# Optimization experiments

Hardware: AMD Instinct MI355X
Metric: run time of the kernel (lower is better)

Reference implementation:

```python
import jax, jax.numpy as jnp
import numpy as np

N_SKILLS = 1024
HIDDEN = 512
BATCH = 64
SEQ = 512
INPUT_DIM = 2 * N_SKILLS


def _lstm_layer(x_tbd, W_ih, W_hh, b_ih, b_hh):
    # x_tbd: [S, B, D_in]; PyTorch gate order: i, f, g, o
    B = x_tbd.shape[1]
    H = W_hh.shape[1]
    h0 = jnp.zeros((B, H), x_tbd.dtype)
    c0 = jnp.zeros((B, H), x_tbd.dtype)

    def step(carry, xt):
        h, c = carry
        gates = xt @ W_ih.T + h @ W_hh.T + (b_ih + b_hh)
        i, f, g, o = jnp.split(gates, 4, axis=-1)
        c_new = jax.nn.sigmoid(f) * c + jax.nn.sigmoid(i) * jnp.tanh(g)
        h_new = jax.nn.sigmoid(o) * jnp.tanh(c_new)
        return (h_new, c_new), h_new

    _, hs = jax.lax.scan(step, (h0, c0), x_tbd)
    return hs  # [S, B, H]


def setup_inputs() -> dict:
    key = jax.random.key(0)
    ks = jax.random.split(key, 12)
    s = 1.0 / np.sqrt(HIDDEN)  # PyTorch LSTM init scale
    inp = {
        "skills": jax.random.randint(ks[0], (BATCH, SEQ), 0, N_SKILLS, dtype=jnp.int32),
        "corrects": jax.random.randint(ks[1], (BATCH, SEQ), 0, 2, dtype=jnp.int32),
        # LSTM layer 0: input_dim = 2*n_skills
        "W_ih0": jax.random.uniform(ks[2], (4 * HIDDEN, INPUT_DIM), jnp.float32, -s, s),
        "W_hh0": jax.random.uniform(ks[3], (4 * HIDDEN, HIDDEN), jnp.float32, -s, s),
        "b_ih0": jax.random.uniform(ks[4], (4 * HIDDEN,), jnp.float32, -s, s),
        "b_hh0": jax.random.uniform(ks[5], (4 * HIDDEN,), jnp.float32, -s, s),
        # LSTM layer 1: input = hidden
        "W_ih1": jax.random.uniform(ks[6], (4 * HIDDEN, HIDDEN), jnp.float32, -s, s),
        "W_hh1": jax.random.uniform(ks[7], (4 * HIDDEN, HIDDEN), jnp.float32, -s, s),
        "b_ih1": jax.random.uniform(ks[8], (4 * HIDDEN,), jnp.float32, -s, s),
        "b_hh1": jax.random.uniform(ks[9], (4 * HIDDEN,), jnp.float32, -s, s),
        # Output projection
        "fc_W": jax.random.uniform(ks[10], (N_SKILLS, HIDDEN), jnp.float32, -s, s),
        "fc_b": jax.random.uniform(ks[11], (N_SKILLS,), jnp.float32, -s, s),
    }
    return inp


def reference(skills, corrects, W_ih0, W_hh0, b_ih0, b_hh0,
              W_ih1, W_hh1, b_ih1, b_hh1, fc_W, fc_b):
    # Vectorized one-hot encoding: index = skill if correct==1 else n_skills+skill
    idx = skills + N_SKILLS * (1 - (corrects == 1).astype(skills.dtype))
    valid = (skills >= 0)
    x = jax.nn.one_hot(idx, INPUT_DIM, dtype=jnp.float32) * valid[..., None]  # [B,S,2n]

    x = jnp.transpose(x, (1, 0, 2))  # [S, B, 2n]
    h1 = _lstm_layer(x, W_ih0, W_hh0, b_ih0, b_hh0)   # [S, B, H]
    h2 = _lstm_layer(h1, W_ih1, W_hh1, b_ih1, b_hh1)  # [S, B, H]
    rnn_out = jnp.transpose(h2, (1, 0, 2))  # [B, S, H]

    # dropout is identity at inference
    logits = rnn_out @ fc_W.T + fc_b  # [B, S, n_skills]
    return jax.nn.sigmoid(logits)
```

## Files before the change

### kernel.cpp

```cpp
#include <hip/hip_runtime.h>
#include <hip/hip_fp16.h>

typedef _Float16 f16;
typedef unsigned int u32;
typedef unsigned long long u64;
typedef _Float16 f16x4 __attribute__((ext_vector_type(4)));
typedef _Float16 f16x8 __attribute__((ext_vector_type(8)));
typedef float f32x4 __attribute__((ext_vector_type(4)));
typedef float f32x16 __attribute__((ext_vector_type(16)));

#define SEQ   512
#define HID   512
#define NSK   1024
#define INDIM 2048
#define G4    2048
#define NWG   64
#define TWORDS 8192

#define H1_OFF    0ull
#define H2_OFF    33554432ull
#define WHH0_OFF  67108864ull
#define WIH1_OFF  69206016ull
#define WHH1_OFF  71303168ull
#define FCW_OFF   73400320ull
#define B0_OFF    74448896ull
#define B1_OFF    74457088ull
#define W0P_OFF   74465280ull
#define FLG_OFF   82853888ull

__device__ __forceinline__ float sigmoidf_(float x) {
    return 1.0f / (1.0f + __expf(-x));
}
__device__ __forceinline__ float tanhf_(float x) {
    return 2.0f * sigmoidf_(2.0f * x) - 1.0f;
}

__device__ __forceinline__ void cstore(u64* p, u64 v) {
    __hip_atomic_store(p, v, __ATOMIC_RELAXED, __HIP_MEMORY_SCOPE_AGENT);
}

__global__ __launch_bounds__(256) void prep_kernel(
    const float* __restrict__ Whh0, const float* __restrict__ Wih1,
    const float* __restrict__ Whh1, const float* __restrict__ fcW,
    const float* __restrict__ bih0, const float* __restrict__ bhh0,
    const float* __restrict__ bih1, const float* __restrict__ bhh1,
    f16* __restrict__ whh0h, f16* __restrict__ wih1h,
    f16* __restrict__ whh1h, f16* __restrict__ fcwh,
    float* __restrict__ b0, float* __restrict__ b1, u32* __restrict__ flags)
{
    int i = blockIdx.x * 256 + threadIdx.x;
    if (i < G4 * HID) {
        whh0h[i] = (f16)Whh0[i];
        wih1h[i] = (f16)Wih1[i];
        whh1h[i] = (f16)Whh1[i];
    }
    if (i < NSK * HID) fcwh[i] = (f16)fcW[i];
    if (i < G4) { b0[i] = bih0[i] + bhh0[i]; b1[i] = bih1[i] + bhh1[i]; }
    if (i < NWG * 16) flags[i] = 0;
}

__global__ __launch_bounds__(256) void w0p_kernel(
    const float* __restrict__ Wih0, f16* __restrict__ w0p)
{
    __shared__ float tl[64][65];
    const int tid = threadIdx.x;
    const int ct = blockIdx.x & 31, rt = blockIdx.x >> 5;
    const int r0 = rt * 64, c0 = ct * 64;
#pragma unroll 4
    for (int i = 0; i < 16; ++i) {
        int rr = i * 4 + (tid >> 6);
        int cc = tid & 63;
        tl[rr][cc] = Wih0[(size_t)(r0 + rr) * INDIM + c0 + cc];
    }
    __syncthreads();
    const int jh = r0 >> 9;
    const int wg0 = (r0 & 511) >> 3;
    for (int task = tid; task < 512; task += 256) {
        int c = task >> 3, wgl = task & 7;
        f16 tmp[8];
#pragma unroll
        for (int jl = 0; jl < 8; ++jl) tmp[jl] = (f16)tl[wgl * 8 + jl][c];
        *(f16x8*)&w0p[(size_t)(c0 + c) * 2048 + (wg0 + wgl) * 32 + jh * 8] =
            *(f16x8*)tmp;
    }
}

struct PArgs {
    const int* skills; const int* corrects;
    const f16* W0P;
    const f16* Whh0; const f16* Wih1; const f16* Whh1;
    const float* b0; const float* b1;
    u64* h1; u64* h2;
    u32* arrive;
};

__global__ __launch_bounds__(256, 1) void lstm_mfma(PArgs a) {
    __shared__ float ex[2 * 2 * 64 * 33];
    __shared__ float bsh[64];

    const int wg   = blockIdx.x;
    const int tid  = threadIdx.x;
    const int lane = tid & 63;
    const int w    = tid >> 6;
    const int ki   = w & 1;
    const int mi   = w >> 1;
    const int u0   = wg * 8;
    const int n    = lane & 31;
    const int nh   = lane >> 5;
    const int rown = (n >> 3) * HID + u0 + (n & 7);
    const int mrow = mi * 32 + (lane & 31);
    const int lyr  = w >> 1;
    const int q    = w & 1;

    if (tid < 64) {
        int l = tid >> 5, nn = tid & 31;
        const float* bb = l ? a.b1 : a.b0;
        bsh[tid] = bb[(nn >> 3) * HID + u0 + (nn & 7)];
    }

    f16x8 Bhh0[16], Bih1[16], Bhh1[16];
#pragma unroll
    for (int f = 0; f < 16; ++f) {
        int k = ki * 256 + f * 16 + nh * 8;
        Bhh0[f] = *(const f16x8*)(a.Whh0 + (size_t)rown * HID + k);
        Bih1[f] = *(const f16x8*)(a.Wih1 + (size_t)rown * HID + k);
        Bhh1[f] = *(const f16x8*)(a.Whh1 + (size_t)rown * HID + k);
    }

    float cst[4];
#pragma unroll
    for (int j = 0; j < 4; ++j) cst[j] = 0.0f;

    uint2 gq0 = {0,0}, gq1 = {0,0}, gq2 = {0,0}, gq3 = {0,0};
    int idxq = -1;
    int sraw = 0, craw = 0;
    if (w < 2) {
        int sk = a.skills[lane * SEQ + 0];
        int co = a.corrects[lane * SEQ + 0];
        idxq = (sk >= 0) ? sk + NSK * ((co == 1) ? 0 : 1) : -1;
        const uint2* gp = (const uint2*)(a.W0P +
            (size_t)((idxq >= 0) ? idxq : 0) * 2048 + wg * 32 + q * 4);
        gq0 = gp[0]; gq1 = gp[2]; gq2 = gp[4]; gq3 = gp[6];
        if (SEQ > 1) {
            sraw = a.skills[lane * SEQ + 1];
            craw = a.corrects[lane * SEQ + 1];
        }
    }

    __syncthreads();

    for (int tau = 0; tau <= SEQ; ++tau) {
        const bool l0 = (tau < SEQ);
        const bool l1 = (tau >= 1);

        union AF { uint4 u; f16x8 v; };
        AF a1[16], a2[16];
        if (l1) {
            const u64* __restrict__ h1p = a.h1 + (size_t)(tau - 1) * TWORDS;
#pragma unroll
            for (int f = 0; f < 16; ++f) {
                int base = (ki * 32 + f * 2 + nh) * 128 + mrow * 2;
                a1[f].u = *(const uint4*)(h1p + base);
            }
        }
        if (tau >= 2) {
            const u64* __restrict__ h2p = a.h2 + (size_t)(tau - 2) * TWORDS;
#pragma unroll
            for (int f = 0; f < 16; ++f) {
                int base = (ki * 32 + f * 2 + nh) * 128 + mrow * 2;
                a2[f].u = *(const uint4*)(h2p + base);
            }
        }

        f32x16 accA, accB;
#pragma unroll
        for (int j = 0; j < 16; ++j) { accA[j] = 0.0f; accB[j] = 0.0f; }

        if (l1) {
            if (l0) {
#pragma unroll
                for (int f = 0; f < 16; ++f)
                    accA = __builtin_amdgcn_mfma_f32_32x32x16_f16(a1[f].v, Bhh0[f], accA, 0, 0, 0);
            }
#pragma unroll
            for (int f = 0; f < 16; ++f)
                accB = __builtin_amdgcn_mfma_f32_32x32x16_f16(a1[f].v, Bih1[f], accB, 0, 0, 0);
        }
        if (tau >= 2) {
#pragma unroll
            for (int f = 0; f < 16; ++f)
                accB = __builtin_amdgcn_mfma_f32_32x32x16_f16(a2[f].v, Bhh1[f], accB, 0, 0, 0);
        }

#pragma unroll
        for (int r = 0; r < 16; ++r) {
            int m = mi * 32 + (r & 3) + 8 * (r >> 2) + 4 * nh;
            ex[(ki * 64 + m) * 33 + n] = accA[r];
            ex[((2 + ki) * 64 + m) * 33 + n] = accB[r];
        }
        __syncthreads();

        const bool cact = lyr ? l1 : l0;
        if (cact) {
            const int t = lyr ? tau - 1 : tau;
            const float* e0 = ex + (lyr * 2 + 0) * (64 * 33) + lane * 33;
            const float* e1 = ex + (lyr * 2 + 1) * (64 * 33) + lane * 33;
            f16 hh[4];
            f16x4 xi = __builtin_bit_cast(f16x4, gq0);
            f16x4 xf = __builtin_bit_cast(f16x4, gq1);
            f16x4 xg = __builtin_bit_cast(f16x4, gq2);
            f16x4 xo = __builtin_bit_cast(f16x4, gq3);
            const bool hasx = (lyr == 0) && (idxq >= 0);
#pragma unroll
            for (int uu = 0; uu < 4; ++uu) {
                int nc = q * 4 + uu;
                float gi = e0[nc]      + e1[nc]      + bsh[lyr * 32 + nc];
                float gf = e0[8 + nc]  + e1[8 + nc]  + bsh[lyr * 32 + 8 + nc];
                float gg = e0[16 + nc] + e1[16 + nc] + bsh[lyr * 32 + 16 + nc];
                float go = e0[24 + nc] + e1[24 + nc] + bsh[lyr * 32 + 24 + nc];
                if (hasx) {
                    gi += (float)xi[uu]; gf += (float)xf[uu];
                    gg += (float)xg[uu]; go += (float)xo[uu];
                }
                float c_ = (t > 0) ? cst[uu] : 0.0f;
                float cn = sigmoidf_(gf) * c_ + sigmoidf_(gi) * tanhf_(gg);
                float hv = sigmoidf_(go) * tanhf_(cn);
                cst[uu] = cn;
                hh[uu] = (f16)hv;
            }
            union HP { f16x4 h; u64 d; } p;
            p.h = (f16x4){hh[0], hh[1], hh[2], hh[3]};
            u64* hb = lyr ? (a.h2 + (size_t)t * TWORDS) : (a.h1 + (size_t)t * TWORDS);
            cstore(hb + (size_t)wg * 128 + lane * 2 + q, p.d);
        }

        if (w < 2 && tau + 1 < SEQ) {
            idxq = (sraw >= 0) ? sraw + NSK * ((craw == 1) ? 0 : 1) : -1;
            const uint2* gp = (const uint2*)(a.W0P +
                (size_t)((idxq >= 0) ? idxq : 0) * 2048 + wg * 32 + q * 4);
            gq0 = gp[0]; gq1 = gp[2]; gq2 = gp[4]; gq3 = gp[6];
            if (tau + 2 < SEQ) {
                sraw = a.skills[lane * SEQ + tau + 2];
                craw = a.corrects[lane * SEQ + tau + 2];
            }
        }

        __syncthreads();
        if (tid == 0)
            __hip_atomic_store(&a.arrive[wg * 16], (u32)(tau + 1), __ATOMIC_RELAXED,
                               __HIP_MEMORY_SCOPE_AGENT);
        if (tau < SEQ) {
            const u32 want = (u32)(tau + 1);
            int guard = 0;
            while (true) {
                u32 v = __hip_atomic_load(&a.arrive[lane * 16], __ATOMIC_RELAXED,
                                          __HIP_MEMORY_SCOPE_AGENT);
                if (__ballot(v < want) == 0ull) break;
                __builtin_amdgcn_s_sleep(1);
                if (++guard > (1 << 20)) break;
            }
            asm volatile("" ::: "memory");
            __builtin_amdgcn_sched_barrier(0);
        }
    }
}

__global__ __launch_bounds__(256) void proj_mfma(
    const u64* __restrict__ h2, const f16* __restrict__ fcwh,
    const float* __restrict__ fcb, float* __restrict__ out)
{
    const int tg = blockIdx.x >> 4;
    const int nt = blockIdx.x & 15;
    const int tid = threadIdx.x;
    const int l = tid & 63;
    const int w = tid >> 6;
    const int col = l & 15;
    const int kb = l >> 4;

    f32x4 acc[4][4];
#pragma unroll
    for (int j = 0; j < 4; ++j)
#pragma unroll
        for (int v = 0; v < 4; ++v) acc[j][v] = (f32x4){0, 0, 0, 0};

    float fb[4];
#pragma unroll
    for (int v = 0; v < 4; ++v) fb[v] = fcb[nt * 64 + v * 16 + col];

    union AF { uint4 u; f16x8 v; };

#pragma unroll 2
    for (int f = 0; f < 16; ++f) {
        f16x8 Bf[4];
#pragma unroll
        for (int v = 0; v < 4; ++v) {
            int nn = nt * 64 + v * 16 + col;
            Bf[v] = *(const f16x8*)(fcwh + (size_t)nn * HID + f * 32 + kb * 8);
        }
#pragma unroll
        for (int j = 0; j < 4; ++j) {
            const u64* hp = h2 + (size_t)(tg * 4 + j) * TWORDS
                          + ((f * 4 + kb) * 128 + (w * 16 + col) * 2);
            AF av; av.u = *(const uint4*)hp;
#pragma unroll
            for (int v = 0; v < 4; ++v)
                acc[j][v] = __builtin_amdgcn_mfma_f32_16x16x32_f16(av.v, Bf[v], acc[j][v], 0, 0, 0);
        }
    }

#pragma unroll
    for (int j = 0; j < 4; ++j) {
        int t = tg * 4 + j;
#pragma unroll
        for (int v = 0; v < 4; ++v) {
            int nn = nt * 64 + v * 16 + col;
#pragma unroll
            for (int r = 0; r < 4; ++r) {
                int b = w * 16 + kb * 4 + r;
                out[((size_t)b * SEQ + t) * NSK + nn] = sigmoidf_(acc[j][v][r] + fb[v]);
            }
        }
    }
}

extern "C" void kernel_launch(void* const* d_in, const int* in_sizes, int n_in,
                              void* d_out, int out_size, void* d_ws, size_t ws_size,
                              hipStream_t stream) {
    (void)in_sizes; (void)n_in; (void)out_size; (void)ws_size;

    const int*   skills   = (const int*)d_in[0];
    const int*   corrects = (const int*)d_in[1];
    const float* Wih0 = (const float*)d_in[2];
    const float* Whh0 = (const float*)d_in[3];
    const float* bih0 = (const float*)d_in[4];
    const float* bhh0 = (const float*)d_in[5];
    const float* Wih1 = (const float*)d_in[6];
    const float* Whh1 = (const float*)d_in[7];
    const float* bih1 = (const float*)d_in[8];
    const float* bhh1 = (const float*)d_in[9];
    const float* fcW  = (const float*)d_in[10];
    const float* fcb  = (const float*)d_in[11];

    char* ws = (char*)d_ws;
    u64*  h1    = (u64*)(ws + H1_OFF);
    u64*  h2    = (u64*)(ws + H2_OFF);
    f16*  whh0h = (f16*)(ws + WHH0_OFF);
    f16*  wih1h = (f16*)(ws + WIH1_OFF);
    f16*  whh1h = (f16*)(ws + WHH1_OFF);
    f16*  fcwh  = (f16*)(ws + FCW_OFF);
    float* b0   = (float*)(ws + B0_OFF);
    float* b1   = (float*)(ws + B1_OFF);
    f16*  w0p   = (f16*)(ws + W0P_OFF);
    u32*  flags = (u32*)(ws + FLG_OFF);

    prep_kernel<<<4096, 256, 0, stream>>>(Whh0, Wih1, Whh1, fcW, bih0, bhh0,
                                          bih1, bhh1, whh0h, wih1h, whh1h, fcwh,
                                          b0, b1, flags);
    w0p_kernel<<<1024, 256, 0, stream>>>(Wih0, w0p);

    PArgs pa;
    pa.skills = skills; pa.corrects = corrects; pa.W0P = w0p;
    pa.Whh0 = whh0h; pa.Wih1 = wih1h; pa.Whh1 = whh1h;
    pa.b0 = b0; pa.b1 = b1; pa.h1 = h1; pa.h2 = h2;
    pa.arrive = flags;

    lstm_mfma<<<NWG, 256, 0, stream>>>(pa);

    proj_mfma<<<2048, 256, 0, stream>>>(h2, fcwh, fcb, (float*)d_out);
}
```

Baseline: 2.678 ms.

## Assign whole K per wave, drop LDS exchange, use per-wave arrival flags

Restructures the persistent LSTM kernel so each wave computes the full K=512 reduction for its layer and batch half. The old split-K LDS exchange and the two __syncthreads per step go away. Gate recombination now uses cross-lane shuffles, and h is stored in a plain [t][b][H] fp16 layout with 16-bit atomic stores. Each wave signals its own arrival flag and the wait polls 256 flags, which drops block-level barriers but doubles per-wave weight registers and makes the stores narrower and more numerous.

```diff
diff --git a/kernel.cpp b/kernel.cpp
--- a/kernel.cpp
+++ b/kernel.cpp
@@ -3,8 +3,8 @@
 
 typedef _Float16 f16;
 typedef unsigned int u32;
+typedef unsigned short u16;
 typedef unsigned long long u64;
-typedef _Float16 f16x4 __attribute__((ext_vector_type(4)));
 typedef _Float16 f16x8 __attribute__((ext_vector_type(8)));
 typedef float f32x4 __attribute__((ext_vector_type(4)));
 typedef float f32x16 __attribute__((ext_vector_type(16)));
@@ -15,7 +15,7 @@
 #define INDIM 2048
 #define G4    2048
 #define NWG   64
-#define TWORDS 8192
+#define HSTEP 32768
 
 #define H1_OFF    0ull
 #define H2_OFF    33554432ull
@@ -35,8 +35,15 @@
     return 2.0f * sigmoidf_(2.0f * x) - 1.0f;
 }
 
-__device__ __forceinline__ void cstore(u64* p, u64 v) {
-    __hip_atomic_store(p, v, __ATOMIC_RELAXED, __HIP_MEMORY_SCOPE_AGENT);
+__device__ __forceinline__ float dot2_(u32 a, u32 b, float c) {
+    typedef _Float16 h2t __attribute__((ext_vector_type(2)));
+    h2t ha = __builtin_bit_cast(h2t, a);
+    h2t hb = __builtin_bit_cast(h2t, b);
+#if __has_builtin(__builtin_amdgcn_fdot2)
+    return __builtin_amdgcn_fdot2(ha, hb, c, false);
+#else
+    return c + (float)ha[0] * (float)hb[0] + (float)ha[1] * (float)hb[1];
+#endif
 }
 
 __global__ __launch_bounds__(256) void prep_kernel(
@@ -56,7 +63,7 @@
     }
     if (i < NSK * HID) fcwh[i] = (f16)fcW[i];
     if (i < G4) { b0[i] = bih0[i] + bhh0[i]; b1[i] = bih1[i] + bhh1[i]; }
-    if (i < NWG * 16) flags[i] = 0;
+    if (i < 4096) flags[i] = 0;
 }
 
 __global__ __launch_bounds__(256) void w0p_kernel(
@@ -90,172 +97,163 @@
     const f16* W0P;
     const f16* Whh0; const f16* Wih1; const f16* Whh1;
     const float* b0; const float* b1;
-    u64* h1; u64* h2;
+    f16* h1; f16* h2;
     u32* arrive;
 };
 
 __global__ __launch_bounds__(256, 1) void lstm_mfma(PArgs a) {
-    __shared__ float ex[2 * 2 * 64 * 33];
-    __shared__ float bsh[64];
-
     const int wg   = blockIdx.x;
     const int tid  = threadIdx.x;
     const int lane = tid & 63;
     const int w    = tid >> 6;
-    const int ki   = w & 1;
-    const int mi   = w >> 1;
+    const int mi   = w & 1;
+    const bool isL1 = (w >= 2);
     const int u0   = wg * 8;
     const int n    = lane & 31;
     const int nh   = lane >> 5;
     const int rown = (n >> 3) * HID + u0 + (n & 7);
-    const int mrow = mi * 32 + (lane & 31);
-    const int lyr  = w >> 1;
-    const int q    = w & 1;
-
-    if (tid < 64) {
-        int l = tid >> 5, nn = tid & 31;
-        const float* bb = l ? a.b1 : a.b0;
-        bsh[tid] = bb[(nn >> 3) * HID + u0 + (nn & 7)];
-    }
-
-    f16x8 Bhh0[16], Bih1[16], Bhh1[16];
-#pragma unroll
-    for (int f = 0; f < 16; ++f) {
-        int k = ki * 256 + f * 16 + nh * 8;
-        Bhh0[f] = *(const f16x8*)(a.Whh0 + (size_t)rown * HID + k);
-        Bih1[f] = *(const f16x8*)(a.Wih1 + (size_t)rown * HID + k);
-        Bhh1[f] = *(const f16x8*)(a.Whh1 + (size_t)rown * HID + k);
-    }
-
-    float cst[4];
-#pragma unroll
-    for (int j = 0; j < 4; ++j) cst[j] = 0.0f;
-
-    uint2 gq0 = {0,0}, gq1 = {0,0}, gq2 = {0,0}, gq3 = {0,0};
-    int idxq = -1;
-    int sraw = 0, craw = 0;
-    if (w < 2) {
-        int sk = a.skills[lane * SEQ + 0];
-        int co = a.corrects[lane * SEQ + 0];
-        idxq = (sk >= 0) ? sk + NSK * ((co == 1) ? 0 : 1) : -1;
-        const uint2* gp = (const uint2*)(a.W0P +
-            (size_t)((idxq >= 0) ? idxq : 0) * 2048 + wg * 32 + q * 4);
-        gq0 = gp[0]; gq1 = gp[2]; gq2 = gp[4]; gq3 = gp[6];
-        if (SEQ > 1) {
-            sraw = a.skills[lane * SEQ + 1];
-            craw = a.corrects[lane * SEQ + 1];
-        }
-    }
-
-    __syncthreads();
+    const int brow = mi * 32 + n;
+
+    const f16* Wb0 = isL1 ? a.Wih1 : a.Whh0;
+    f16x8 B0[32], B1[32];
+#pragma unroll
+    for (int f = 0; f < 32; ++f)
+        B0[f] = *(const f16x8*)(Wb0 + (size_t)rown * HID + f * 16 + nh * 8);
+    if (isL1) {
+#pragma unroll
+        for (int f = 0; f < 32; ++f)
+            B1[f] = *(const f16x8*)(a.Whh1 + (size_t)rown * HID + f * 16 + nh * 8);
+    }
+    const float biasv = (isL1 ? a.b1 : a.b0)[rown];
+
+    float cst[16];
+#pragma unroll
+    for (int r = 0; r < 16; ++r) cst[r] = 0.0f;
+
+    u16 xv[16];
+#pragma unroll
+    for (int r = 0; r < 16; ++r) xv[r] = 0;
+    if (!isL1) {
+#pragma unroll
+        for (int r = 0; r < 16; ++r) {
+            int b = mi * 32 + (r & 3) + 8 * (r >> 2) + 4 * nh;
+            int sk = a.skills[b * SEQ + 0];
+            int co = a.corrects[b * SEQ + 0];
+            if (sk >= 0) {
+                int idx = sk + NSK * ((co == 1) ? 0 : 1);
+                xv[r] = *(const u16*)(a.W0P + (size_t)idx * 2048 + wg * 32 + n);
+            }
+        }
+    }
+
+    const int s8  = (lane & 32) | ((n + 8) & 31);
+    const int s16 = (lane & 32) | ((n + 16) & 31);
+    const int s24 = (lane & 32) | ((n + 24) & 31);
 
     for (int tau = 0; tau <= SEQ; ++tau) {
-        const bool l0 = (tau < SEQ);
-        const bool l1 = (tau >= 1);
-
-        union AF { uint4 u; f16x8 v; };
-        AF a1[16], a2[16];
-        if (l1) {
-            const u64* __restrict__ h1p = a.h1 + (size_t)(tau - 1) * TWORDS;
-#pragma unroll
-            for (int f = 0; f < 16; ++f) {
-                int base = (ki * 32 + f * 2 + nh) * 128 + mrow * 2;
-                a1[f].u = *(const uint4*)(h1p + base);
-            }
-        }
-        if (tau >= 2) {
-            const u64* __restrict__ h2p = a.h2 + (size_t)(tau - 2) * TWORDS;
-#pragma unroll
-            for (int f = 0; f < 16; ++f) {
-                int base = (ki * 32 + f * 2 + nh) * 128 + mrow * 2;
-                a2[f].u = *(const uint4*)(h2p + base);
-            }
-        }
-
-        f32x16 accA, accB;
-#pragma unroll
-        for (int j = 0; j < 16; ++j) { accA[j] = 0.0f; accB[j] = 0.0f; }
-
-        if (l1) {
-            if (l0) {
-#pragma unroll
-                for (int f = 0; f < 16; ++f)
-                    accA = __builtin_amdgcn_mfma_f32_32x32x16_f16(a1[f].v, Bhh0[f], accA, 0, 0, 0);
-            }
-#pragma unroll
-            for (int f = 0; f < 16; ++f)
-                accB = __builtin_amdgcn_mfma_f32_32x32x16_f16(a1[f].v, Bih1[f], accB, 0, 0, 0);
-        }
-        if (tau >= 2) {
-#pragma unroll
-            for (int f = 0; f < 16; ++f)
-                accB = __builtin_amdgcn_mfma_f32_32x32x16_f16(a2[f].v, Bhh1[f], accB, 0, 0, 0);
-        }
-
-#pragma unroll
-        for (int r = 0; r < 16; ++r) {
-            int m = mi * 32 + (r & 3) + 8 * (r >> 2) + 4 * nh;
-            ex[(ki * 64 + m) * 33 + n] = accA[r];
-            ex[((2 + ki) * 64 + m) * 33 + n] = accB[r];
-        }
-        __syncthreads();
-
-        const bool cact = lyr ? l1 : l0;
-        if (cact) {
-            const int t = lyr ? tau - 1 : tau;
-            const float* e0 = ex + (lyr * 2 + 0) * (64 * 33) + lane * 33;
-            const float* e1 = ex + (lyr * 2 + 1) * (64 * 33) + lane * 33;
-            f16 hh[4];
-            f16x4 xi = __builtin_bit_cast(f16x4, gq0);
-            f16x4 xf = __builtin_bit_cast(f16x4, gq1);
-            f16x4 xg = __builtin_bit_cast(f16x4, gq2);
-            f16x4 xo = __builtin_bit_cast(f16x4, gq3);
-            const bool hasx = (lyr == 0) && (idxq >= 0);
-#pragma unroll
-            for (int uu = 0; uu < 4; ++uu) {
-                int nc = q * 4 + uu;
-                float gi = e0[nc]      + e1[nc]      + bsh[lyr * 32 + nc];
-                float gf = e0[8 + nc]  + e1[8 + nc]  + bsh[lyr * 32 + 8 + nc];
-                float gg = e0[16 + nc] + e1[16 + nc] + bsh[lyr * 32 + 16 + nc];
-                float go = e0[24 + nc] + e1[24 + nc] + bsh[lyr * 32 + 24 + nc];
-                if (hasx) {
-                    gi += (float)xi[uu]; gf += (float)xf[uu];
-                    gg += (float)xg[uu]; go += (float)xo[uu];
+        const bool active = isL1 ? (tau >= 1) : (tau < SEQ);
+        if (active) {
+            const int t = isL1 ? tau - 1 : tau;
+
+            f32x16 acc;
+#pragma unroll
+            for (int j = 0; j < 16; ++j) acc[j] = 0.0f;
+
+            uint4 af[32];
+            if (!isL1) {
+                if (tau >= 1) {
+                    const f16* hp = a.h1 + (size_t)(tau - 1) * HSTEP
+                                  + (size_t)brow * HID + nh * 8;
+#pragma unroll
+                    for (int f = 0; f < 32; ++f) af[f] = *(const uint4*)(hp + f * 16);
+#pragma unroll
+                    for (int f = 0; f < 32; ++f)
+                        acc = __builtin_amdgcn_mfma_f32_32x32x16_f16(
+                            __builtin_bit_cast(f16x8, af[f]), B0[f], acc, 0, 0, 0);
                 }
-                float c_ = (t > 0) ? cst[uu] : 0.0f;
-                float cn = sigmoidf_(gf) * c_ + sigmoidf_(gi) * tanhf_(gg);
-                float hv = sigmoidf_(go) * tanhf_(cn);
-                cst[uu] = cn;
-                hh[uu] = (f16)hv;
-            }
-            union HP { f16x4 h; u64 d; } p;
-            p.h = (f16x4){hh[0], hh[1], hh[2], hh[3]};
-            u64* hb = lyr ? (a.h2 + (size_t)t * TWORDS) : (a.h1 + (size_t)t * TWORDS);
-            cstore(hb + (size_t)wg * 128 + lane * 2 + q, p.d);
-        }
-
-        if (w < 2 && tau + 1 < SEQ) {
-            idxq = (sraw >= 0) ? sraw + NSK * ((craw == 1) ? 0 : 1) : -1;
-            const uint2* gp = (const uint2*)(a.W0P +
-                (size_t)((idxq >= 0) ? idxq : 0) * 2048 + wg * 32 + q * 4);
-            gq0 = gp[0]; gq1 = gp[2]; gq2 = gp[4]; gq3 = gp[6];
-            if (tau + 2 < SEQ) {
-                sraw = a.skills[lane * SEQ + tau + 2];
-                craw = a.corrects[lane * SEQ + tau + 2];
-            }
-        }
-
-        __syncthreads();
-        if (tid == 0)
-            __hip_atomic_store(&a.arrive[wg * 16], (u32)(tau + 1), __ATOMIC_RELAXED,
-                               __HIP_MEMORY_SCOPE_AGENT);
+            } else {
+                const f16* hp1 = a.h1 + (size_t)(tau - 1) * HSTEP
+                               + (size_t)brow * HID + nh * 8;
+#pragma unroll
+                for (int f = 0; f < 32; ++f) af[f] = *(const uint4*)(hp1 + f * 16);
+#pragma unroll
+                for (int f = 0; f < 32; ++f)
+                    acc = __builtin_amdgcn_mfma_f32_32x32x16_f16(
+                        __builtin_bit_cast(f16x8, af[f]), B0[f], acc, 0, 0, 0);
+                if (tau >= 2) {
+                    const f16* hp2 = a.h2 + (size_t)(tau - 2) * HSTEP
+                                   + (size_t)brow * HID + nh * 8;
+#pragma unroll
+                    for (int f = 0; f < 32; ++f) af[f] = *(const uint4*)(hp2 + f * 16);
+#pragma unroll
+                    for (int f = 0; f < 32; ++f)
+                        acc = __builtin_amdgcn_mfma_f32_32x32x16_f16(
+                            __builtin_bit_cast(f16x8, af[f]), B1[f], acc, 0, 0, 0);
+                }
+            }
+
+            float pre[16];
+#pragma unroll
+            for (int r = 0; r < 16; ++r) {
+                pre[r] = acc[r] + biasv;
+                if (!isL1)
+                    pre[r] += (float)__builtin_bit_cast(f16, xv[r]);
+            }
+
+            f16* hb = (isL1 ? a.h2 : a.h1) + (size_t)t * HSTEP + (u0 + n);
+            const bool usec = isL1 ? (tau >= 2) : (tau >= 1);
+#pragma unroll
+            for (int r = 0; r < 16; ++r) {
+                float pf = __shfl(pre[r], s8, 64);
+                float pg = __shfl(pre[r], s16, 64);
+                float po = __shfl(pre[r], s24, 64);
+                if (n < 8) {
+                    float c_ = usec ? cst[r] : 0.0f;
+                    float cn = sigmoidf_(pf) * c_ + sigmoidf_(pre[r]) * tanhf_(pg);
+                    float hv = sigmoidf_(po) * tanhf_(cn);
+                    cst[r] = cn;
+                    int b = mi * 32 + (r & 3) + 8 * (r >> 2) + 4 * nh;
+                    __hip_atomic_store((u16*)(hb + (size_t)b * HID),
+                                       __builtin_bit_cast(u16, (f16)hv),
+                                       __ATOMIC_RELAXED, __HIP_MEMORY_SCOPE_AGENT);
+                }
+            }
+        }
+
         if (tau < SEQ) {
+            asm volatile("s_waitcnt vmcnt(0)" ::: "memory");
+            if (lane == 0)
+                __hip_atomic_store(&a.arrive[(wg * 4 + w) * 16], (u32)(tau + 1),
+                                   __ATOMIC_RELAXED, __HIP_MEMORY_SCOPE_AGENT);
+
+            if (!isL1 && tau + 1 < SEQ) {
+#pragma unroll
+                for (int r = 0; r < 16; ++r) {
+                    int b = mi * 32 + (r & 3) + 8 * (r >> 2) + 4 * nh;
+                    int sk = a.skills[b * SEQ + tau + 1];
+                    int co = a.corrects[b * SEQ + tau + 1];
+                    u16 v = 0;
+                    if (sk >= 0) {
+                        int idx = sk + NSK * ((co == 1) ? 0 : 1);
+                        v = *(const u16*)(a.W0P + (size_t)idx * 2048 + wg * 32 + n);
+                    }
+                    xv[r] = v;
+                }
+            }
+
             const u32 want = (u32)(tau + 1);
             int guard = 0;
             while (true) {
-                u32 v = __hip_atomic_load(&a.arrive[lane * 16], __ATOMIC_RELAXED,
-                                          __HIP_MEMORY_SCOPE_AGENT);
-                if (__ballot(v < want) == 0ull) break;
+                u32 v0 = __hip_atomic_load(&a.arrive[(lane) * 16],
+                                           __ATOMIC_RELAXED, __HIP_MEMORY_SCOPE_AGENT);
+                u32 v1 = __hip_atomic_load(&a.arrive[(lane + 64) * 16],
+                                           __ATOMIC_RELAXED, __HIP_MEMORY_SCOPE_AGENT);
+                u32 v2 = __hip_atomic_load(&a.arrive[(lane + 128) * 16],
+                                           __ATOMIC_RELAXED, __HIP_MEMORY_SCOPE_AGENT);
+                u32 v3 = __hip_atomic_load(&a.arrive[(lane + 192) * 16],
+                                           __ATOMIC_RELAXED, __HIP_MEMORY_SCOPE_AGENT);
+                u32 mn = min(min(v0, v1), min(v2, v3));
+                if (__ballot(mn < want) == 0ull) break;
                 __builtin_amdgcn_s_sleep(1);
                 if (++guard > (1 << 20)) break;
             }
@@ -266,7 +264,7 @@
 }
 
 __global__ __launch_bounds__(256) void proj_mfma(
-    const u64* __restrict__ h2, const f16* __restrict__ fcwh,
+    const f16* __restrict__ h2, const f16* __restrict__ fcwh,
     const float* __restrict__ fcb, float* __restrict__ out)
 {
     const int tg = blockIdx.x >> 4;
@@ -287,8 +285,6 @@
 #pragma unroll
     for (int v = 0; v < 4; ++v) fb[v] = fcb[nt * 64 + v * 16 + col];
 
-    union AF { uint4 u; f16x8 v; };
-
 #pragma unroll 2
     for (int f = 0; f < 16; ++f) {
         f16x8 Bf[4];
@@ -299,12 +295,13 @@
         }
 #pragma unroll
         for (int j = 0; j < 4; ++j) {
-            const u64* hp = h2 + (size_t)(tg * 4 + j) * TWORDS
-                          + ((f * 4 + kb) * 128 + (w * 16 + col) * 2);
-            AF av; av.u = *(const uint4*)hp;
+            const f16* hp = h2 + (size_t)(tg * 4 + j) * HSTEP
+                          + (size_t)(w * 16 + col) * HID + f * 32 + kb * 8;
+            uint4 au = *(const uint4*)hp;
 #pragma unroll
             for (int v = 0; v < 4; ++v)
-                acc[j][v] = __builtin_amdgcn_mfma_f32_16x16x32_f16(av.v, Bf[v], acc[j][v], 0, 0, 0);
+                acc[j][v] = __builtin_amdgcn_mfma_f32_16x16x32_f16(
+                    __builtin_bit_cast(f16x8, au), Bf[v], acc[j][v], 0, 0, 0);
         }
     }
 
@@ -342,8 +339,8 @@
     const float* fcb  = (const float*)d_in[11];
 
     char* ws = (char*)d_ws;
-    u64*  h1    = (u64*)(ws + H1_OFF);
-    u64*  h2    = (u64*)(ws + H2_OFF);
+    f16*  h1    = (f16*)(ws + H1_OFF);
+    f16*  h2    = (f16*)(ws + H2_OFF);
     f16*  whh0h = (f16*)(ws + WHH0_OFF);
     f16*  wih1h = (f16*)(ws + WIH1_OFF);
     f16*  whh1h = (f16*)(ws + WHH1_OFF);
```

After: 9.464 ms. 253% more time.
